# Optimization experiments

Hardware: AMD Instinct MI355X
Metric: run time of the kernel (lower is better)

The kernel has to match this reference:

```python
import jax, jax.numpy as jnp
import numpy as np

B, S, D, H, DK = 8, 1024, 768, 12, 64


def setup_inputs() -> dict:
    key = jax.random.key(0)
    k1, k2, k3, k4, k5 = jax.random.split(key, 5)
    return {
        "x": jax.random.normal(k1, (B, S, D), dtype=jnp.float32),
        "Wq": jax.random.normal(k2, (H, D, DK), dtype=jnp.float32),
        "Wk": jax.random.normal(k3, (H, D, DK), dtype=jnp.float32),
        "Wv": jax.random.normal(k4, (H, D, DK), dtype=jnp.float32),
        "W": jax.random.normal(k5, (D, D), dtype=jnp.float32),
    }


def reference(x, Wq, Wk, Wv, W):
    # Batched equivalent of the per-head SelfAttention loop + concat + W matmul.
    q = jnp.einsum("bsd,hdk->bhsk", x, Wq)  # [B,H,S,DK]
    k = jnp.einsum("bsd,hdk->bhsk", x, Wk)
    v = jnp.einsum("bsd,hdk->bhsk", x, Wv)
    scale = 1.0 / jnp.sqrt(jnp.asarray(DK, dtype=x.dtype))
    scores = jnp.einsum("bhsk,bhtk->bhst", q, k) * scale  # [B,H,S,S]
    attn = jax.nn.softmax(scores, axis=-1)
    z = jnp.einsum("bhst,bhtk->bhsk", attn, v)  # [B,H,S,DK]
    # concat heads along last dim: [B,S,H*DK]
    z = jnp.transpose(z, (0, 2, 1, 3)).reshape(x.shape[0], x.shape[1], H * DK)
    return jnp.matmul(z, W)  # [B,S,D]
```

## Files before the change

### kernel.cpp

```cpp
#include <hip/hip_runtime.h>

#define Bv 8
#define Sv 1024
#define Dv 768
#define Hv 12
#define DKv 64
#define Mv (Bv*Sv)
#define NQKV (3*Hv*DKv)
#define NQK (2*Hv*DKv)

typedef __attribute__((ext_vector_type(8))) short short8;
typedef __attribute__((ext_vector_type(4))) float f32x4;

__device__ __forceinline__ short f2bf(float f) {
    unsigned u = __builtin_bit_cast(unsigned, f);
    u += 0x7fffu + ((u >> 16) & 1u);
    return (short)(u >> 16);
}
__device__ __forceinline__ float bf2f(short h) {
    return __builtin_bit_cast(float, (unsigned)(unsigned short)h << 16);
}

__device__ __forceinline__ f32x4 mfma16(short8 a, short8 b, f32x4 c) {
    return __builtin_amdgcn_mfma_f32_16x16x32_bf16(a, b, c, 0, 0, 0);
}

__device__ __forceinline__ void gload16(const short* g, const short* l) {
    __builtin_amdgcn_global_load_lds(
        (const __attribute__((address_space(1))) unsigned int*)g,
        (__attribute__((address_space(3))) unsigned int*)(short*)l, 16, 0, 0);
}

__global__ void split_x_kernel(const float* __restrict__ x, short* __restrict__ xh,
                               short* __restrict__ xl) {
    int t = blockIdx.x * 256 + threadIdx.x;
    const float4* f = (const float4*)x + (size_t)t * 2;
    float4 a = f[0], b = f[1];
    float v[8] = {a.x,a.y,a.z,a.w,b.x,b.y,b.z,b.w};
    short8 oh, ol;
#pragma unroll
    for (int k = 0; k < 8; k++) {
        short hi = f2bf(v[k]);
        oh[k] = hi;
        ol[k] = f2bf(v[k] - bf2f(hi));
    }
    *((short8*)xh + t) = oh;
    *((short8*)xl + t) = ol;
}

__global__ void pack_wqkv_kernel(const float* __restrict__ Wq, const float* __restrict__ Wk,
                                 const float* __restrict__ Wv, short* __restrict__ Wh,
                                 short* __restrict__ Wl) {
    int dt = blockIdx.x;
    int h  = blockIdx.y;
    int p  = blockIdx.z;
    const float* S = (p == 0 ? Wq : (p == 1 ? Wk : Wv)) + (size_t)h * Dv * DKv;
    float sc = (p == 0) ? 0.125f : 1.0f;
    __shared__ float lds[64][65];
    int t = threadIdx.x;
    int d0 = dt * 64;
#pragma unroll
    for (int i = 0; i < 4; i++) {
        int v = t + i * 256;
        int r = v >> 4, c4 = v & 15;
        float4 f = *(const float4*)&S[(size_t)(d0 + r) * DKv + c4 * 4];
        lds[r][c4*4+0] = f.x; lds[r][c4*4+1] = f.y; lds[r][c4*4+2] = f.z; lds[r][c4*4+3] = f.w;
    }
    __syncthreads();
#pragma unroll
    for (int i = 0; i < 2; i++) {
        int v = t + i * 256;
        int kk = v >> 3, dl0 = (v & 7) * 8;
        short8 oh, ol;
#pragma unroll
        for (int k = 0; k < 8; k++) {
            float f = lds[dl0 + k][kk] * sc;
            short hi = f2bf(f);
            oh[k] = hi;
            ol[k] = f2bf(f - bf2f(hi));
        }
        size_t base = (size_t)(p*768 + h*64 + kk) * Dv + d0 + dl0;
        *(short8*)&Wh[base] = oh;
        if (p < 2) *(short8*)&Wl[base] = ol;
    }
}

__global__ void transpose_cast_kernel(const float* __restrict__ S, int S_cols,
                                      short* __restrict__ D, int D_ld) {
    int c0 = blockIdx.x * 64, r0 = blockIdx.y * 64;
    __shared__ float lds[64][65];
    int t = threadIdx.x;
#pragma unroll
    for (int i = 0; i < 4; i++) {
        int v = t + i * 256;
        int r = v >> 4, c4 = v & 15;
        float4 f = *(const float4*)&S[(size_t)(r0 + r) * S_cols + c0 + c4 * 4];
        lds[r][c4*4+0] = f.x; lds[r][c4*4+1] = f.y; lds[r][c4*4+2] = f.z; lds[r][c4*4+3] = f.w;
    }
    __syncthreads();
#pragma unroll
    for (int i = 0; i < 2; i++) {
        int v = t + i * 256;
        int oc = v >> 3, rl0 = (v & 7) * 8;
        short8 o;
#pragma unroll
        for (int k = 0; k < 8; k++) o[k] = f2bf(lds[rl0 + k][oc]);
        *(short8*)&D[(size_t)(c0 + oc) * D_ld + r0 + rl0] = o;
    }
}

__global__ void vtrans_kernel(const short* __restrict__ QKVh, short* __restrict__ Vt) {
    int sc = blockIdx.x;
    int bh = blockIdx.y;
    int b = bh / Hv, h = bh % Hv;
    __shared__ __align__(16) short lds[64][72];
    int t = threadIdx.x;
    int s0 = sc * 64;
#pragma unroll
    for (int i = 0; i < 2; i++) {
        int v = t + i * 256;
        int sl = v >> 3, c0 = (v & 7) * 8;
        short8 xv = *(const short8*)&QKVh[(size_t)(b*Sv + s0 + sl) * NQKV + NQK + h*DKv + c0];
        *(short8*)&lds[sl][c0] = xv;
    }
    __syncthreads();
#pragma unroll
    for (int i = 0; i < 2; i++) {
        int v = t + i * 256;
        int dk = v >> 3, tl0 = (v & 7) * 8;
        short8 o;
#pragma unroll
        for (int k = 0; k < 8; k++) o[k] = lds[tl0 + k][dk];
        *(short8*)&Vt[(size_t)(bh*64 + dk) * Sv + s0 + tl0] = o;
    }
}

__device__ __forceinline__ void swz_xy(int n, int& xbl, int& ybl) {
    int cx = n & 7, k = n >> 3;
    ybl = cx + 8 * (k & 7);
    xbl = k >> 3;
}

__global__ __launch_bounds__(256) void gemm1_kernel(const short* __restrict__ xh,
                                                    const short* __restrict__ xl,
                                                    const short* __restrict__ Wh,
                                                    const short* __restrict__ Wl,
                                                    short* __restrict__ QKVh,
                                                    short* __restrict__ QKVl) {
    int xbl, ybl;
    swz_xy(blockIdx.x, xbl, ybl);
    int m0 = ybl * 128, n0 = xbl * 128;
    bool isv = (n0 >= NQK);
    __shared__ __align__(16) short lAh[128 * 32];
    __shared__ __align__(16) short lAl[128 * 32];
    __shared__ __align__(16) short lBh[128 * 32];
    __shared__ __align__(16) short lBl[128 * 32];
    int tid = threadIdx.x, lane = tid & 63, w = tid >> 6;
    int wr = w >> 1, wc = w & 1;
    int li = lane & 15, g = lane >> 4;
    f32x4 zero = {0.f, 0.f, 0.f, 0.f};
    f32x4 acc[4][4];
#pragma unroll
    for (int i = 0; i < 4; i++)
#pragma unroll
        for (int j = 0; j < 4; j++) acc[i][j] = zero;

    int e0 = w * 512 + lane * 8;
    int r0 = e0 >> 5, c0 = e0 & 31;
    int e1 = e0 + 2048;
    int r1 = e1 >> 5, c1 = e1 & 31;

    for (int k0 = 0; k0 < Dv; k0 += 32) {
        __syncthreads();
        gload16(xh + (size_t)(m0 + r0) * Dv + k0 + c0, &lAh[w * 512]);
        gload16(xh + (size_t)(m0 + r1) * Dv + k0 + c1, &lAh[2048 + w * 512]);
        gload16(Wh + (size_t)(n0 + r0) * Dv + k0 + c0, &lBh[w * 512]);
        gload16(Wh + (size_t)(n0 + r1) * Dv + k0 + c1, &lBh[2048 + w * 512]);
        if (!isv) {
            gload16(xl + (size_t)(m0 + r0) * Dv + k0 + c0, &lAl[w * 512]);
            gload16(xl + (size_t)(m0 + r1) * Dv + k0 + c1, &lAl[2048 + w * 512]);
            gload16(Wl + (size_t)(n0 + r0) * Dv + k0 + c0, &lBl[w * 512]);
            gload16(Wl + (size_t)(n0 + r1) * Dv + k0 + c1, &lBl[2048 + w * 512]);
        }
        __syncthreads();
        short8 ah[4], bh[4];
#pragma unroll
        for (int mi = 0; mi < 4; mi++)
            ah[mi] = *(const short8*)&lAh[(wr*64 + mi*16 + li) * 32 + g * 8];
#pragma unroll
        for (int ni = 0; ni < 4; ni++)
            bh[ni] = *(const short8*)&lBh[(wc*64 + ni*16 + li) * 32 + g * 8];
        if (isv) {
#pragma unroll
            for (int mi = 0; mi < 4; mi++)
#pragma unroll
                for (int ni = 0; ni < 4; ni++)
                    acc[mi][ni] = mfma16(ah[mi], bh[ni], acc[mi][ni]);
        } else {
            short8 al[4], bl[4];
#pragma unroll
            for (int mi = 0; mi < 4; mi++)
                al[mi] = *(const short8*)&lAl[(wr*64 + mi*16 + li) * 32 + g * 8];
#pragma unroll
            for (int ni = 0; ni < 4; ni++)
                bl[ni] = *(const short8*)&lBl[(wc*64 + ni*16 + li) * 32 + g * 8];
#pragma unroll
            for (int mi = 0; mi < 4; mi++)
#pragma unroll
                for (int ni = 0; ni < 4; ni++) {
                    acc[mi][ni] = mfma16(ah[mi], bh[ni], acc[mi][ni]);
                    acc[mi][ni] = mfma16(ah[mi], bl[ni], acc[mi][ni]);
                    acc[mi][ni] = mfma16(al[mi], bh[ni], acc[mi][ni]);
                }
        }
    }
#pragma unroll
    for (int mi = 0; mi < 4; mi++)
#pragma unroll
        for (int ni = 0; ni < 4; ni++)
#pragma unroll
            for (int j = 0; j < 4; j++) {
                int row = m0 + wr*64 + mi*16 + g*4 + j;
                int col = n0 + wc*64 + ni*16 + li;
                float v = acc[mi][ni][j];
                short hi = f2bf(v);
                QKVh[(size_t)row * NQKV + col] = hi;
                if (!isv) QKVl[(size_t)row * NQK + col] = f2bf(v - bf2f(hi));
            }
}

__global__ __launch_bounds__(256) void gemm2_kernel(const short* __restrict__ A,
                                                    const short* __restrict__ Bt,
                                                    float* __restrict__ C) {
    int xbl, ybl;
    swz_xy(blockIdx.x, xbl, ybl);
    int m0 = ybl * 128, n0 = xbl * 128;
    __shared__ __align__(16) short lA[128 * 32];
    __shared__ __align__(16) short lB[128 * 32];
    int tid = threadIdx.x, lane = tid & 63, w = tid >> 6;
    int wr = w >> 1, wc = w & 1;
    int li = lane & 15, g = lane >> 4;
    f32x4 zero = {0.f, 0.f, 0.f, 0.f};
    f32x4 acc[4][4];
#pragma unroll
    for (int i = 0; i < 4; i++)
#pragma unroll
        for (int j = 0; j < 4; j++) acc[i][j] = zero;

    int e0 = w * 512 + lane * 8;
    int r0 = e0 >> 5, c0 = e0 & 31;
    int e1 = e0 + 2048;
    int r1 = e1 >> 5, c1 = e1 & 31;

    for (int k0 = 0; k0 < Dv; k0 += 32) {
        __syncthreads();
        gload16(A  + (size_t)(m0 + r0) * Dv + k0 + c0, &lA[w * 512]);
        gload16(A  + (size_t)(m0 + r1) * Dv + k0 + c1, &lA[2048 + w * 512]);
        gload16(Bt + (size_t)(n0 + r0) * Dv + k0 + c0, &lB[w * 512]);
        gload16(Bt + (size_t)(n0 + r1) * Dv + k0 + c1, &lB[2048 + w * 512]);
        __syncthreads();
        short8 a[4], bb[4];
#pragma unroll
        for (int mi = 0; mi < 4; mi++)
            a[mi] = *(const short8*)&lA[(wr*64 + mi*16 + li) * 32 + g * 8];
#pragma unroll
        for (int ni = 0; ni < 4; ni++)
            bb[ni] = *(const short8*)&lB[(wc*64 + ni*16 + li) * 32 + g * 8];
#pragma unroll
        for (int mi = 0; mi < 4; mi++)
#pragma unroll
            for (int ni = 0; ni < 4; ni++)
                acc[mi][ni] = mfma16(a[mi], bb[ni], acc[mi][ni]);
    }
#pragma unroll
    for (int mi = 0; mi < 4; mi++)
#pragma unroll
        for (int ni = 0; ni < 4; ni++)
#pragma unroll
            for (int j = 0; j < 4; j++) {
                int row = m0 + wr*64 + mi*16 + g*4 + j;
                int col = n0 + wc*64 + ni*16 + li;
                C[(size_t)row * Dv + col] = acc[mi][ni][j];
            }
}

__global__ __launch_bounds__(512, 6) void attn_kernel(const short* __restrict__ QKVh,
                                                      const short* __restrict__ QKVl,
                                                      const short* __restrict__ Vt,
                                                      short* __restrict__ Z) {
    int n = blockIdx.x;
    int j2 = n >> 3;
    int bh = (n & 7) + 8 * (j2 >> 3);
    int qb = j2 & 7;
    int b = bh / Hv, h = bh % Hv;
    int tid = threadIdx.x, lane = tid & 63, w = tid >> 6;
    int li = lane & 15, g = lane >> 4;

    __shared__ __align__(16) short Kh[64 * 64];
    __shared__ __align__(16) short Kl[64 * 64];
    __shared__ __align__(16) short Vs[64 * 64];
    __shared__ __align__(16) short P[8][1024];
    char* Pw = (char*)&P[w][0];
    const char* Khc = (const char*)Kh;
    const char* Klc = (const char*)Kl;
    const char* Vsc = (const char*)Vs;

    int qr0 = qb * 128 + w * 16;
    const short* qhr = QKVh + (size_t)(b*Sv + qr0 + li) * NQKV + h * DKv;
    const short* qlr = QKVl + (size_t)(b*Sv + qr0 + li) * NQK  + h * DKv;
    short8 qh0 = *(const short8*)(qhr + g * 8);
    short8 qh1 = *(const short8*)(qhr + 32 + g * 8);
    short8 ql0 = *(const short8*)(qlr + g * 8);
    short8 ql1 = *(const short8*)(qlr + 32 + g * 8);

    const short* Khb = QKVh + (size_t)(b*Sv) * NQKV + Hv*DKv + h*DKv;
    const short* Klb = QKVl + (size_t)(b*Sv) * NQK  + Hv*DKv + h*DKv;
    const short* Vbase = Vt + (size_t)(bh * 64) * Sv;

    int srow = w * 8 + (lane >> 3);
    int scs  = (lane & 7) ^ (srow & 7);

    float mm = -1e30f, ll = 0.f;
    f32x4 zero = {0.f, 0.f, 0.f, 0.f};
    f32x4 acc[4];
#pragma unroll
    for (int ni = 0; ni < 4; ni++) acc[ni] = zero;

    for (int t = 0; t < 16; t++) {
        int t0 = t * 64;
        gload16(Khb + (size_t)(t0 + srow) * NQKV + scs * 8, &Kh[w * 512]);
        gload16(Klb + (size_t)(t0 + srow) * NQK  + scs * 8, &Kl[w * 512]);
        gload16(Vbase + (size_t)srow * Sv + t0 + scs * 8,   &Vs[w * 512]);
        __syncthreads();

        f32x4 s[4];
#pragma unroll
        for (int tn = 0; tn < 4; tn++) {
            int row = tn * 16 + li;
            int rb = row * 128, rs = (row & 7) << 4;
            short8 kh0 = *(const short8*)(Khc + rb + ((g << 4) ^ rs));
            short8 kh1 = *(const short8*)(Khc + rb + ((64 + (g << 4)) ^ rs));
            short8 kl0 = *(const short8*)(Klc + rb + ((g << 4) ^ rs));
            short8 kl1 = *(const short8*)(Klc + rb + ((64 + (g << 4)) ^ rs));
            f32x4 z = mfma16(kh0, qh0, zero);
            z = mfma16(kh1, qh1, z);
            z = mfma16(kl0, qh0, z);
            z = mfma16(kl1, qh1, z);
            z = mfma16(kh0, ql0, z);
            z = mfma16(kh1, ql1, z);
            s[tn] = z;
        }
        float rm = s[0][0];
#pragma unroll
        for (int tn = 0; tn < 4; tn++)
#pragma unroll
            for (int jj = 0; jj < 4; jj++) rm = fmaxf(rm, s[tn][jj]);
        rm = fmaxf(rm, __shfl_xor(rm, 16));
        rm = fmaxf(rm, __shfl_xor(rm, 32));
        float mn = fmaxf(mm, rm);
        float sfu = __expf(mm - mn);
        float p[4][4];
        float rs2 = 0.f;
#pragma unroll
        for (int tn = 0; tn < 4; tn++)
#pragma unroll
            for (int jj = 0; jj < 4; jj++) { p[tn][jj] = __expf(s[tn][jj] - mn); rs2 += p[tn][jj]; }
        rs2 += __shfl_xor(rs2, 16);
        rs2 += __shfl_xor(rs2, 32);
        ll = ll * sfu + rs2;
        mm = mn;

        float sfq[4];
#pragma unroll
        for (int jj = 0; jj < 4; jj++) sfq[jj] = __shfl(sfu, g * 4 + jj);
#pragma unroll
        for (int ni = 0; ni < 4; ni++)
#pragma unroll
            for (int jj = 0; jj < 4; jj++) acc[ni][jj] *= sfq[jj];

#pragma unroll
        for (int tn = 0; tn < 4; tn++) {
            unsigned lo, hi;
            asm("v_cvt_pk_bf16_f32 %0, %1, %2" : "=v"(lo) : "v"(p[tn][0]), "v"(p[tn][1]));
            asm("v_cvt_pk_bf16_f32 %0, %1, %2" : "=v"(hi) : "v"(p[tn][2]), "v"(p[tn][3]));
            unsigned long long pk = (unsigned long long)lo | ((unsigned long long)hi << 32);
            int off = (li * 128 + tn * 32 + g * 8) ^ ((li & 7) << 4);
            *(unsigned long long*)(Pw + off) = pk;
        }
#pragma unroll
        for (int kt = 0; kt < 2; kt++) {
            int roff = (li * 128 + kt * 64 + g * 16) ^ ((li & 7) << 4);
            short8 ap = *(const short8*)(Pw + roff);
#pragma unroll
            for (int ni = 0; ni < 4; ni++) {
                int dk = ni * 16 + li;
                int vb = dk * 128 + ((((kt * 4 + g) << 4)) ^ ((dk & 7) << 4));
                short8 bv = *(const short8*)(Vsc + vb);
                acc[ni] = mfma16(ap, bv, acc[ni]);
            }
        }
        __syncthreads();
    }
    float inv = 1.f / ll;
    float invq[4];
#pragma unroll
    for (int jj = 0; jj < 4; jj++) invq[jj] = __shfl(inv, g * 4 + jj);
#pragma unroll
    for (int ni = 0; ni < 4; ni++)
#pragma unroll
        for (int jj = 0; jj < 4; jj++) {
            int row = b*Sv + qr0 + g*4 + jj;
            int col = h*DKv + ni*16 + li;
            Z[(size_t)row * Dv + col] = f2bf(acc[ni][jj] * invq[jj]);
        }
}

extern "C" void kernel_launch(void* const* d_in, const int* in_sizes, int n_in,
                              void* d_out, int out_size, void* d_ws, size_t ws_size,
                              hipStream_t stream) {
    const float* x  = (const float*)d_in[0];
    const float* Wq = (const float*)d_in[1];
    const float* Wk = (const float*)d_in[2];
    const float* Wv = (const float*)d_in[3];
    const float* W  = (const float*)d_in[4];
    float* out = (float*)d_out;

    short* xh   = (short*)d_ws;
    short* xl   = xh   + (size_t)Mv * Dv;
    short* Wh   = xl   + (size_t)Mv * Dv;
    short* Wl   = Wh   + (size_t)NQKV * Dv;
    short* W2T  = Wl   + (size_t)NQKV * Dv;
    short* QKVh = W2T  + (size_t)Dv * Dv;
    short* QKVl = QKVh + (size_t)Mv * NQKV;
    short* Vt   = QKVl + (size_t)Mv * NQK;
    short* Zb   = Vt   + (size_t)Bv*Hv*DKv * Sv;

    split_x_kernel<<<dim3(Mv * Dv / (256 * 8)), 256, 0, stream>>>(x, xh, xl);
    pack_wqkv_kernel<<<dim3(Dv/64, Hv, 3), 256, 0, stream>>>(Wq, Wk, Wv, Wh, Wl);
    transpose_cast_kernel<<<dim3(Dv/64, Dv/64), 256, 0, stream>>>(W, Dv, W2T, Dv);
    gemm1_kernel<<<dim3((NQKV/128) * (Mv/128)), 256, 0, stream>>>(xh, xl, Wh, Wl, QKVh, QKVl);
    vtrans_kernel<<<dim3(Sv/64, Bv*Hv), 256, 0, stream>>>(QKVh, Vt);
    attn_kernel<<<dim3(768), 512, 0, stream>>>(QKVh, QKVl, Vt, Zb);
    gemm2_kernel<<<dim3((Dv/128) * (Mv/128)), 256, 0, stream>>>(Zb, W2T, out);
}
```

Before: 217.6 us.

## Double-buffer LDS in projection GEMMs with swizzled layout and flattened split-bf16 loop

Both projection GEMMs now use two LDS buffers, so the global-to-LDS load of the next K tile is issued before the MFMAs on the current tile, with one barrier per step instead of two. LDS columns are XOR-swizzled by row to reduce bank conflicts on the short8 fragment reads. In gemm1 the three-product hi/lo split is flattened into one 72-step K loop over (xh,Wh),(xh,Wl),(xl,Wh) segments with a single buffer set, instead of loading four tiles per step. The aim is to hide load latency and improve occupancy via launch bounds of 4 blocks; the cost is that the swizzle and staging logic must stay correct, and the accumulation order changes.

```diff
diff --git a/kernel.cpp b/kernel.cpp
--- a/kernel.cpp
+++ b/kernel.cpp
@@ -141,20 +141,19 @@
     xbl = k >> 3;
 }
 
-__global__ __launch_bounds__(256) void gemm1_kernel(const short* __restrict__ xh,
-                                                    const short* __restrict__ xl,
-                                                    const short* __restrict__ Wh,
-                                                    const short* __restrict__ Wl,
-                                                    short* __restrict__ QKVh,
-                                                    short* __restrict__ QKVl) {
+__global__ __launch_bounds__(256, 4) void gemm1_kernel(const short* __restrict__ xh,
+                                                       const short* __restrict__ xl,
+                                                       const short* __restrict__ Wh,
+                                                       const short* __restrict__ Wl,
+                                                       short* __restrict__ QKVh,
+                                                       short* __restrict__ QKVl) {
     int xbl, ybl;
     swz_xy(blockIdx.x, xbl, ybl);
     int m0 = ybl * 128, n0 = xbl * 128;
     bool isv = (n0 >= NQK);
-    __shared__ __align__(16) short lAh[128 * 32];
-    __shared__ __align__(16) short lAl[128 * 32];
-    __shared__ __align__(16) short lBh[128 * 32];
-    __shared__ __align__(16) short lBl[128 * 32];
+    int KT = isv ? 24 : 72;
+    __shared__ __align__(16) short lA[2][4096];
+    __shared__ __align__(16) short lB[2][4096];
     int tid = threadIdx.x, lane = tid & 63, w = tid >> 6;
     int wr = w >> 1, wc = w & 1;
     int li = lane & 15, g = lane >> 4;
@@ -165,54 +164,50 @@
 #pragma unroll
         for (int j = 0; j < 4; j++) acc[i][j] = zero;
 
-    int e0 = w * 512 + lane * 8;
-    int r0 = e0 >> 5, c0 = e0 & 31;
-    int e1 = e0 + 2048;
-    int r1 = e1 >> 5, c1 = e1 & 31;
-
-    for (int k0 = 0; k0 < Dv; k0 += 32) {
-        __syncthreads();
-        gload16(xh + (size_t)(m0 + r0) * Dv + k0 + c0, &lAh[w * 512]);
-        gload16(xh + (size_t)(m0 + r1) * Dv + k0 + c1, &lAh[2048 + w * 512]);
-        gload16(Wh + (size_t)(n0 + r0) * Dv + k0 + c0, &lBh[w * 512]);
-        gload16(Wh + (size_t)(n0 + r1) * Dv + k0 + c1, &lBh[2048 + w * 512]);
-        if (!isv) {
-            gload16(xl + (size_t)(m0 + r0) * Dv + k0 + c0, &lAl[w * 512]);
-            gload16(xl + (size_t)(m0 + r1) * Dv + k0 + c1, &lAl[2048 + w * 512]);
-            gload16(Wl + (size_t)(n0 + r0) * Dv + k0 + c0, &lBl[w * 512]);
-            gload16(Wl + (size_t)(n0 + r1) * Dv + k0 + c1, &lBl[2048 + w * 512]);
-        }
-        __syncthreads();
-        short8 ah[4], bh[4];
+    int e0 = tid * 8;
+    int sr0 = e0 >> 5;
+    int sc0 = ((e0 >> 3) & 3) ^ ((sr0 >> 1) & 3);
+    int sr1 = sr0 + 64;
+    int sc1 = ((e0 >> 3) & 3) ^ ((sr1 >> 1) & 3);
+
+    auto stage = [&](int t, int buf) {
+        int seg = (t >= 48) ? 2 : (t >= 24 ? 1 : 0);
+        int kk = (t - seg * 24) * 32;
+        const short* Ab = (seg == 2) ? xl : xh;
+        const short* Bb = (seg == 1) ? Wl : Wh;
+        gload16(Ab + (size_t)(m0 + sr0) * Dv + kk + sc0 * 8, &lA[buf][w * 512]);
+        gload16(Bb + (size_t)(n0 + sr0) * Dv + kk + sc0 * 8, &lB[buf][w * 512]);
+        gload16(Ab + (size_t)(m0 + sr1) * Dv + kk + sc1 * 8, &lA[buf][2048 + w * 512]);
+        gload16(Bb + (size_t)(n0 + sr1) * Dv + kk + sc1 * 8, &lB[buf][2048 + w * 512]);
+    };
+
+    stage(0, 0);
+    asm volatile("s_waitcnt vmcnt(0)" ::: "memory");
+    __builtin_amdgcn_s_barrier();
+
+    for (int t = 0; t < KT; t++) {
+        int cur = t & 1;
+        if (t + 1 < KT) stage(t + 1, cur ^ 1);
+        __builtin_amdgcn_sched_barrier(0);
+        short8 a[4], bb[4];
+#pragma unroll
+        for (int mi = 0; mi < 4; mi++) {
+            int row = wr*64 + mi*16 + li;
+            a[mi] = *(const short8*)&lA[cur][row * 32 + ((g ^ ((row >> 1) & 3)) << 3)];
+        }
+#pragma unroll
+        for (int ni = 0; ni < 4; ni++) {
+            int row = wc*64 + ni*16 + li;
+            bb[ni] = *(const short8*)&lB[cur][row * 32 + ((g ^ ((row >> 1) & 3)) << 3)];
+        }
 #pragma unroll
         for (int mi = 0; mi < 4; mi++)
-            ah[mi] = *(const short8*)&lAh[(wr*64 + mi*16 + li) * 32 + g * 8];
-#pragma unroll
-        for (int ni = 0; ni < 4; ni++)
-            bh[ni] = *(const short8*)&lBh[(wc*64 + ni*16 + li) * 32 + g * 8];
-        if (isv) {
-#pragma unroll
-            for (int mi = 0; mi < 4; mi++)
-#pragma unroll
-                for (int ni = 0; ni < 4; ni++)
-                    acc[mi][ni] = mfma16(ah[mi], bh[ni], acc[mi][ni]);
-        } else {
-            short8 al[4], bl[4];
-#pragma unroll
-            for (int mi = 0; mi < 4; mi++)
-                al[mi] = *(const short8*)&lAl[(wr*64 + mi*16 + li) * 32 + g * 8];
 #pragma unroll
             for (int ni = 0; ni < 4; ni++)
-                bl[ni] = *(const short8*)&lBl[(wc*64 + ni*16 + li) * 32 + g * 8];
-#pragma unroll
-            for (int mi = 0; mi < 4; mi++)
-#pragma unroll
-                for (int ni = 0; ni < 4; ni++) {
-                    acc[mi][ni] = mfma16(ah[mi], bh[ni], acc[mi][ni]);
-                    acc[mi][ni] = mfma16(ah[mi], bl[ni], acc[mi][ni]);
-                    acc[mi][ni] = mfma16(al[mi], bh[ni], acc[mi][ni]);
-                }
-        }
+                acc[mi][ni] = mfma16(a[mi], bb[ni], acc[mi][ni]);
+        asm volatile("s_waitcnt vmcnt(0)" ::: "memory");
+        __builtin_amdgcn_s_barrier();
+        __builtin_amdgcn_sched_barrier(0);
     }
 #pragma unroll
     for (int mi = 0; mi < 4; mi++)
@@ -229,14 +224,14 @@
             }
 }
 
-__global__ __launch_bounds__(256) void gemm2_kernel(const short* __restrict__ A,
-                                                    const short* __restrict__ Bt,
-                                                    float* __restrict__ C) {
+__global__ __launch_bounds__(256, 4) void gemm2_kernel(const short* __restrict__ A,
+                                                       const short* __restrict__ Bt,
+                                                       float* __restrict__ C) {
     int xbl, ybl;
     swz_xy(blockIdx.x, xbl, ybl);
     int m0 = ybl * 128, n0 = xbl * 128;
-    __shared__ __align__(16) short lA[128 * 32];
-    __shared__ __align__(16) short lB[128 * 32];
+    __shared__ __align__(16) short lA[2][4096];
+    __shared__ __align__(16) short lB[2][4096];
     int tid = threadIdx.x, lane = tid & 63, w = tid >> 6;
     int wr = w >> 1, wc = w & 1;
     int li = lane & 15, g = lane >> 4;
@@ -247,30 +242,47 @@
 #pragma unroll
         for (int j = 0; j < 4; j++) acc[i][j] = zero;
 
-    int e0 = w * 512 + lane * 8;
-    int r0 = e0 >> 5, c0 = e0 & 31;
-    int e1 = e0 + 2048;
-    int r1 = e1 >> 5, c1 = e1 & 31;
-
-    for (int k0 = 0; k0 < Dv; k0 += 32) {
-        __syncthreads();
-        gload16(A  + (size_t)(m0 + r0) * Dv + k0 + c0, &lA[w * 512]);
-        gload16(A  + (size_t)(m0 + r1) * Dv + k0 + c1, &lA[2048 + w * 512]);
-        gload16(Bt + (size_t)(n0 + r0) * Dv + k0 + c0, &lB[w * 512]);
-        gload16(Bt + (size_t)(n0 + r1) * Dv + k0 + c1, &lB[2048 + w * 512]);
-        __syncthreads();
+    int e0 = tid * 8;
+    int sr0 = e0 >> 5;
+    int sc0 = ((e0 >> 3) & 3) ^ ((sr0 >> 1) & 3);
+    int sr1 = sr0 + 64;
+    int sc1 = ((e0 >> 3) & 3) ^ ((sr1 >> 1) & 3);
+
+    auto stage = [&](int t, int buf) {
+        int kk = t * 32;
+        gload16(A  + (size_t)(m0 + sr0) * Dv + kk + sc0 * 8, &lA[buf][w * 512]);
+        gload16(Bt + (size_t)(n0 + sr0) * Dv + kk + sc0 * 8, &lB[buf][w * 512]);
+        gload16(A  + (size_t)(m0 + sr1) * Dv + kk + sc1 * 8, &lA[buf][2048 + w * 512]);
+        gload16(Bt + (size_t)(n0 + sr1) * Dv + kk + sc1 * 8, &lB[buf][2048 + w * 512]);
+    };
+
+    stage(0, 0);
+    asm volatile("s_waitcnt vmcnt(0)" ::: "memory");
+    __builtin_amdgcn_s_barrier();
+
+    for (int t = 0; t < 24; t++) {
+        int cur = t & 1;
+        if (t + 1 < 24) stage(t + 1, cur ^ 1);
+        __builtin_amdgcn_sched_barrier(0);
         short8 a[4], bb[4];
 #pragma unroll
-        for (int mi = 0; mi < 4; mi++)
-            a[mi] = *(const short8*)&lA[(wr*64 + mi*16 + li) * 32 + g * 8];
-#pragma unroll
-        for (int ni = 0; ni < 4; ni++)
-            bb[ni] = *(const short8*)&lB[(wc*64 + ni*16 + li) * 32 + g * 8];
+        for (int mi = 0; mi < 4; mi++) {
+            int row = wr*64 + mi*16 + li;
+            a[mi] = *(const short8*)&lA[cur][row * 32 + ((g ^ ((row >> 1) & 3)) << 3)];
+        }
+#pragma unroll
+        for (int ni = 0; ni < 4; ni++) {
+            int row = wc*64 + ni*16 + li;
+            bb[ni] = *(const short8*)&lB[cur][row * 32 + ((g ^ ((row >> 1) & 3)) << 3)];
+        }
 #pragma unroll
         for (int mi = 0; mi < 4; mi++)
 #pragma unroll
             for (int ni = 0; ni < 4; ni++)
                 acc[mi][ni] = mfma16(a[mi], bb[ni], acc[mi][ni]);
+        asm volatile("s_waitcnt vmcnt(0)" ::: "memory");
+        __builtin_amdgcn_s_barrier();
+        __builtin_amdgcn_sched_barrier(0);
     }
 #pragma unroll
     for (int mi = 0; mi < 4; mi++)
```

After: 202.6 us. 6.9% less time.
